# Performance work log

Measured on AMD Instinct MI355X. Metric: run time of the kernel, lower is better.

The kernel has to match this reference:

```python
import jax, jax.numpy as jnp
import numpy as np

# --- static config / quantization scales (simulating the torch-int modules) ---
B, S, E, H = 2, 2048, 2048, 16
D = E // H  # head_dim = 128
CATTN_ALPHA = 0.004   # W8A8B8O8Conv1D requant scale: int32 acc -> int8 out
QK_ALPHA = 1e-4       # BMM_S8T_S8N_F32T: s_q * s_k dequant scale -> fp32 logits
PV_ALPHA = 0.002      # BMM_S8T_S8N_S8T: (1/127)*s_v/s_out requant scale -> int8 out
PROJ_ALPHA = 0.003    # W8A8BFP32OFP32Conv1D dequant scale -> fp32 out


def q8(x):
    """round + saturate to int8 range (values kept in float32)."""
    return jnp.clip(jnp.round(x), -128.0, 127.0)


def setup_inputs() -> dict:
    key = jax.random.key(0)
    k0, k1, k2, k3, k4 = jax.random.split(key, 5)
    i8 = lambda k, shape: jax.random.randint(k, shape, -128, 128).astype(jnp.float32)
    return {
        "hidden_states": i8(k0, (B, S, E)),      # int8 activations (simulated)
        "w_attn": i8(k1, (E, 3 * E)),            # int8 c_attn weight (Conv1D: x @ W)
        "b_attn": i8(k2, (3 * E,)),              # int8 c_attn bias
        "w_proj": i8(k3, (E, E)),                # int8 c_proj weight
        "b_proj": jax.random.normal(k4, (E,), dtype=jnp.float32),  # fp32 c_proj bias
    }


def reference(hidden_states, w_attn, b_attn, w_proj, b_proj):
    # c_attn: W8A8B8O8 — int32 accumulate, requantize, add int8 bias, saturate
    qkv = q8(CATTN_ALPHA * jnp.matmul(hidden_states, w_attn) + b_attn)  # [B,S,3E] int8
    q, k, v = jnp.split(qkv, 3, axis=-1)

    def split_heads(t):  # [B,S,E] -> [B,H,S,D]
        return t.reshape(B, S, H, D).transpose(0, 2, 1, 3)

    q, k, v = split_heads(q), split_heads(k), split_heads(v)

    # qk_bmm: BMM_S8T_S8N_F32T -> fp32 logits, then /sqrt(head_dim)
    logits = QK_ALPHA * jnp.einsum("bhqd,bhkd->bhqk", q, k)
    logits = logits / jnp.float32(np.sqrt(D))

    # causal mask (tril bias buffer); masked positions -> dtype min
    causal = jnp.tril(jnp.ones((S, S), dtype=bool))
    mask_value = jnp.finfo(logits.dtype).min
    logits = jnp.where(causal[None, None], logits, mask_value)

    # softmax, then requantize probabilities to int8: round(p * 127)
    p = jax.nn.softmax(logits, axis=-1)
    p_i8 = q8(p * 127.0)  # [B,H,S,S] int8 (simulated)

    # pv_bmm: BMM_S8T_S8N_S8T -> int8 attn output
    attn_out = q8(PV_ALPHA * jnp.einsum("bhqk,bhkd->bhqd", p_i8, v))  # [B,H,S,D]

    # merge heads -> [B,S,E]
    attn_out = attn_out.transpose(0, 2, 1, 3).reshape(B, S, E)

    # c_proj: W8A8BFP32OFP32 — int32 accumulate, dequant to fp32, add fp32 bias
    out = PROJ_ALPHA * jnp.matmul(attn_out, w_proj) + b_proj  # [B,S,E] fp32
    return out
```

## Files before the change

### kernel.cpp

```cpp
#include <hip/hip_runtime.h>
#include <cstdint>
#include <cstddef>


typedef int v4i __attribute__((ext_vector_type(4)));

static constexpr float CATTN_ALPHA = 0.004f;
static constexpr float PV_ALPHA    = 0.002f;
static constexpr float PROJ_ALPHA  = 0.003f;
static constexpr float CE2   = 1.275174308e-05f;
static constexpr float MAGIC = 12582912.0f;

#define GLL16(gp, lp)                                              \
  __builtin_amdgcn_global_load_lds(                                \
      (const __attribute__((address_space(1))) void*)(gp),         \
      (__attribute__((address_space(3))) void*)(lp), 16, 0, 0)

__device__ __forceinline__ float exp2_fast(float x) {
#if __has_builtin(__builtin_amdgcn_exp2f)
  return __builtin_amdgcn_exp2f(x);
#else
  return __builtin_exp2f(x);
#endif
}

__device__ __forceinline__ uint32_t pack4(uint32_t u0, uint32_t u1, uint32_t u2,
                                          uint32_t u3) {
#if __has_builtin(__builtin_amdgcn_perm)
  uint32_t t01 = __builtin_amdgcn_perm(u1, u0, 0x00000400u);
  uint32_t t23 = __builtin_amdgcn_perm(u3, u2, 0x00000400u);
  return __builtin_amdgcn_perm(t23, t01, 0x05040100u);
#else
  return (u0 & 255u) | ((u1 & 255u) << 8) | ((u2 & 255u) << 16) | (u3 << 24);
#endif
}

__device__ __forceinline__ uint32_t rq8(float alpha, int a, float b) {
  float f = __fadd_rn(__fmul_rn(alpha, (float)a), b);
  f = rintf(f);
  f = fminf(fmaxf(f, -128.f), 127.f);
  return (uint32_t)((int)f) & 255u;
}

__global__ __launch_bounds__(256) void quant_kernel(const float* __restrict__ src,
                                                    int8_t* __restrict__ dst, int n4) {
  int i = blockIdx.x * 256 + threadIdx.x;
  if (i >= n4) return;
  float4 v = reinterpret_cast<const float4*>(src)[i];
  int b0 = __float2int_rn(v.x) & 255;
  int b1 = __float2int_rn(v.y) & 255;
  int b2 = __float2int_rn(v.z) & 255;
  int b3 = __float2int_rn(v.w) & 255;
  reinterpret_cast<int*>(dst)[i] = b0 | (b1 << 8) | (b2 << 16) | (b3 << 24);
}

__global__ __launch_bounds__(256) void quant_transpose_kernel(const float* __restrict__ src,
                                                              int8_t* __restrict__ dst,
                                                              int K, int N) {
  __shared__ int8_t ts[64][68];
  const int k0 = blockIdx.x * 64, n0 = blockIdx.y * 64;
  const int t = threadIdx.x;
  for (int c = t; c < 1024; c += 256) {
    int r = c >> 4, cc = (c & 15) << 2;
    float4 v = *reinterpret_cast<const float4*>(&src[(size_t)(k0 + r) * N + n0 + cc]);
    int b0 = __float2int_rn(v.x) & 255;
    int b1 = __float2int_rn(v.y) & 255;
    int b2 = __float2int_rn(v.z) & 255;
    int b3 = __float2int_rn(v.w) & 255;
    *reinterpret_cast<int*>(&ts[r][cc]) = b0 | (b1 << 8) | (b2 << 16) | (b3 << 24);
  }
  __syncthreads();
  {
    int c = t;
    int rn = c >> 2, ck = (c & 3) << 4;
    __attribute__((aligned(16))) int8_t tmp[16];
#pragma unroll
    for (int j = 0; j < 16; ++j) tmp[j] = ts[ck + j][rn];
    *reinterpret_cast<v4i*>(&dst[(size_t)(n0 + rn) * K + k0 + ck]) =
        *reinterpret_cast<const v4i*>(tmp);
  }
}

__global__ __launch_bounds__(256) void gemm_cattn_kernel(
    const int8_t* __restrict__ A, const int8_t* __restrict__ BT,
    const float* __restrict__ bias,
    int8_t* __restrict__ qout, int8_t* __restrict__ kout, int8_t* __restrict__ vtout) {
  __shared__ __align__(16) int8_t As[2][128][64];
  __shared__ __align__(16) int8_t Bs[2][128][64];
  const int t = threadIdx.x;
  const int lane = t & 63, wave = t >> 6;
  const int wr = wave >> 1, wc = wave & 1;
  const int l15 = lane & 15, l4 = lane >> 4;
  const int m0 = blockIdx.y * 128, n0 = blockIdx.x * 128;

  const int srow = lane >> 2;
  const int scol = (((lane & 3) ^ ((lane >> 3) & 3)) << 4);
  const int8_t* ag = A + (size_t)(m0 + wave * 32 + srow) * 2048 + scol;
  const int8_t* bg = BT + (size_t)(n0 + wave * 32 + srow) * 2048 + scol;

  auto stage = [&](int b, int ki) {
    const int8_t* a_ = ag + ki * 64;
    GLL16(a_, &As[b][wave * 32][0]);
    GLL16(a_ + (size_t)16 * 2048, &As[b][wave * 32 + 16][0]);
    const int8_t* b_ = bg + ki * 64;
    GLL16(b_, &Bs[b][wave * 32][0]);
    GLL16(b_ + (size_t)16 * 2048, &Bs[b][wave * 32 + 16][0]);
  };

  v4i acc[4][4];
#pragma unroll
  for (int i = 0; i < 4; ++i)
#pragma unroll
    for (int j = 0; j < 4; ++j) acc[i][j] = (v4i){0, 0, 0, 0};

  const int rsz = ((l4 ^ ((l15 >> 1) & 3)) << 4);
  const int aoff = (wr * 64 + l15) * 64 + rsz;
  const int boff = (wc * 64 + l15) * 64 + rsz;

  stage(0, 0);
  for (int ki = 0; ki < 32; ++ki) {
    if (ki < 31) {
      stage((ki + 1) & 1, ki + 1);
      asm volatile("s_waitcnt vmcnt(4)" ::: "memory");
    } else {
      asm volatile("s_waitcnt vmcnt(0)" ::: "memory");
    }
    __builtin_amdgcn_sched_barrier(0);
    __builtin_amdgcn_s_barrier();
    __builtin_amdgcn_sched_barrier(0);
    const int8_t* ab = &As[ki & 1][0][0];
    const int8_t* bb = &Bs[ki & 1][0][0];
    v4i af[4], bf[4];
#pragma unroll
    for (int i = 0; i < 4; ++i)
      af[i] = *reinterpret_cast<const v4i*>(ab + aoff + i * 1024);
#pragma unroll
    for (int j = 0; j < 4; ++j)
      bf[j] = *reinterpret_cast<const v4i*>(bb + boff + j * 1024);
#pragma unroll
    for (int i = 0; i < 4; ++i)
#pragma unroll
      for (int j = 0; j < 4; ++j)
        acc[i][j] = __builtin_amdgcn_mfma_i32_16x16x64_i8(af[i], bf[j], acc[i][j], 0, 0, 0);
    __builtin_amdgcn_sched_barrier(0);
    __builtin_amdgcn_s_barrier();
  }

  const int which = n0 >> 11;
  const int hh = (n0 & 2047) >> 7;
  const int bi = m0 >> 11;
  const int s_base = m0 & 2047;
  float bv[4];
#pragma unroll
  for (int j = 0; j < 4; ++j) bv[j] = bias[n0 + wc * 64 + j * 16 + l15];

  if (which == 2) {
    int8_t* vb = vtout + ((size_t)(bi * 16 + hh) * 128) * 2048;
#pragma unroll
    for (int i = 0; i < 4; ++i) {
#pragma unroll
      for (int j = 0; j < 4; ++j) {
        uint32_t w = pack4(rq8(CATTN_ALPHA, acc[i][j][0], bv[j]),
                           rq8(CATTN_ALPHA, acc[i][j][1], bv[j]),
                           rq8(CATTN_ALPHA, acc[i][j][2], bv[j]),
                           rq8(CATTN_ALPHA, acc[i][j][3], bv[j]));
        int d = wc * 64 + j * 16 + l15;
        int s0i = s_base + wr * 64 + i * 16 + l4 * 4;
        *reinterpret_cast<uint32_t*>(vb + (size_t)d * 2048 + s0i) = w;
      }
    }
  } else {
    int8_t* dst = (which == 0) ? qout : kout;
    int8_t* db = dst + ((size_t)(bi * 16 + hh) * 2048 + s_base) * 128;
#pragma unroll
    for (int i = 0; i < 4; ++i)
#pragma unroll
      for (int j = 0; j < 4; ++j)
#pragma unroll
        for (int rr = 0; rr < 4; ++rr) {
          float f = __fadd_rn(__fmul_rn(CATTN_ALPHA, (float)acc[i][j][rr]), bv[j]);
          f = rintf(f);
          f = fminf(fmaxf(f, -128.f), 127.f);
          int mo = wr * 64 + i * 16 + l4 * 4 + rr;
          int d = wc * 64 + j * 16 + l15;
          db[(size_t)mo * 128 + d] = (int8_t)(int)f;
        }
  }
}

__global__ __launch_bounds__(256) void gemm_cproj_kernel(
    const int8_t* __restrict__ A, const int8_t* __restrict__ BT,
    const float* __restrict__ bias, float* __restrict__ out) {
  __shared__ __align__(16) int8_t As[2][128][128];
  __shared__ __align__(16) int8_t Bs[2][128][128];
  const int t = threadIdx.x;
  const int lane = t & 63, wave = t >> 6;
  const int wr = wave >> 1, wc = wave & 1;
  const int l15 = lane & 15, l4 = lane >> 4;
  const int m0 = blockIdx.y * 128, n0 = blockIdx.x * 128;

  const int srow = lane >> 3;
  const int scol = ((lane & 7) ^ srow) << 4;
  const int8_t* ag = A + (size_t)(m0 + wave * 32 + srow) * 2048 + scol;
  const int8_t* bg = BT + (size_t)(n0 + wave * 32 + srow) * 2048 + scol;

  auto stage = [&](int b, int ki) {
    const int8_t* a_ = ag + ki * 128;
    const int8_t* b_ = bg + ki * 128;
#pragma unroll
    for (int g = 0; g < 4; ++g) {
      GLL16(a_ + (size_t)(g * 8) * 2048, &As[b][wave * 32 + g * 8][0]);
      GLL16(b_ + (size_t)(g * 8) * 2048, &Bs[b][wave * 32 + g * 8][0]);
    }
  };

  v4i acc[4][4];
#pragma unroll
  for (int i = 0; i < 4; ++i)
#pragma unroll
    for (int j = 0; j < 4; ++j) acc[i][j] = (v4i){0, 0, 0, 0};

  const int rswz = (l4 ^ (l15 & 7)) << 4;
  const int aoff = (wr * 64 + l15) * 128 + rswz;
  const int boff = (wc * 64 + l15) * 128 + rswz;

  stage(0, 0);
  for (int ki = 0; ki < 16; ++ki) {
    if (ki < 15) {
      stage((ki + 1) & 1, ki + 1);
      asm volatile("s_waitcnt vmcnt(8)" ::: "memory");
    } else {
      asm volatile("s_waitcnt vmcnt(0)" ::: "memory");
    }
    __builtin_amdgcn_sched_barrier(0);
    __builtin_amdgcn_s_barrier();
    __builtin_amdgcn_sched_barrier(0);
    const int8_t* ab = &As[ki & 1][0][0];
    const int8_t* bb = &Bs[ki & 1][0][0];
#pragma unroll
    for (int ks = 0; ks < 2; ++ks) {
      v4i af[4], bf[4];
#pragma unroll
      for (int i = 0; i < 4; ++i)
        af[i] = *reinterpret_cast<const v4i*>(ab + ((aoff + i * 2048) ^ (ks * 64)));
#pragma unroll
      for (int j = 0; j < 4; ++j)
        bf[j] = *reinterpret_cast<const v4i*>(bb + ((boff + j * 2048) ^ (ks * 64)));
#pragma unroll
      for (int i = 0; i < 4; ++i)
#pragma unroll
        for (int j = 0; j < 4; ++j)
          acc[i][j] = __builtin_amdgcn_mfma_i32_16x16x64_i8(bf[j], af[i], acc[i][j], 0, 0, 0);
    }
    __builtin_amdgcn_sched_barrier(0);
    __builtin_amdgcn_s_barrier();
  }
#pragma unroll
  for (int j = 0; j < 4; ++j) {
    float4 b4 = *reinterpret_cast<const float4*>(&bias[n0 + wc * 64 + j * 16 + l4 * 4]);
#pragma unroll
    for (int i = 0; i < 4; ++i) {
      int m = m0 + wr * 64 + i * 16 + l15;
      int n = n0 + wc * 64 + j * 16 + l4 * 4;
      float4 o;
      o.x = __fadd_rn(__fmul_rn(PROJ_ALPHA, (float)acc[i][j][0]), b4.x);
      o.y = __fadd_rn(__fmul_rn(PROJ_ALPHA, (float)acc[i][j][1]), b4.y);
      o.z = __fadd_rn(__fmul_rn(PROJ_ALPHA, (float)acc[i][j][2]), b4.z);
      o.w = __fadd_rn(__fmul_rn(PROJ_ALPHA, (float)acc[i][j][3]), b4.w);
      *reinterpret_cast<float4*>(&out[(size_t)m * 2048 + n]) = o;
    }
  }
}

__global__ __launch_bounds__(256) void attn_kernel(
    const int8_t* __restrict__ Q, const int8_t* __restrict__ K8,
    const int8_t* __restrict__ VT, int8_t* __restrict__ O) {
  __shared__ __align__(16) int8_t q_s[64][128];
  __shared__ __align__(16) int8_t k_s[2][64][128];
  __shared__ __align__(16) int8_t vt_s[2][128][64];
  __shared__ __align__(16) int8_t p_s[64][80];

  const int t = threadIdx.x;
  const int lane = t & 63, wave = t >> 6;
  const int l15 = lane & 15, l4 = lane >> 4;
  const int bh = blockIdx.x;
  const int qt = (int)gridDim.y - 1 - (int)blockIdx.y;
  const int r0 = qt * 64;
  const size_t kqbase = (size_t)bh * (2048 * 128);
  const size_t vtbase = (size_t)bh * (128 * 2048);

  const int kq_go = ((lane >> 3) << 7) + ((((lane & 7) ^ (lane >> 3)) & 7) << 4);
  const int vt_go = ((lane >> 2) * 2048) + ((lane & 3) << 4);
  const int koff0 = (l15 << 7) + ((((0 + l4) ^ l15) & 7) << 4);
  const int koff1 = (l15 << 7) + ((((4 + l4) ^ l15) & 7) << 4);
  const int voff = l15 * 64 + l4 * 16;
  const int poff_w = (wave * 16 + l15) * 80 + l4 * 4;
  const int poff_r = (wave * 16 + l15) * 80 + l4 * 16;

  {
    const int8_t* qg = Q + kqbase + (size_t)(r0 + wave * 16) * 128 + kq_go;
    GLL16(qg, &q_s[wave * 16][0]);
    GLL16(qg + 8 * 128, &q_s[wave * 16 + 8][0]);
    const int8_t* kg = K8 + kqbase + (size_t)(wave * 16) * 128 + kq_go;
    GLL16(kg, &k_s[0][wave * 16][0]);
    GLL16(kg + 8 * 128, &k_s[0][wave * 16 + 8][0]);
  }
  __syncthreads();

  const v4i qf0 = *reinterpret_cast<const v4i*>(&q_s[0][0] + wave * 2048 + koff0);
  const v4i qf1 = *reinterpret_cast<const v4i*>(&q_s[0][0] + wave * 2048 + koff1);
  const int qgl = wave * 16 + l15;

  float acc_l[4] = {0.f, 0.f, 0.f, 0.f};

  for (int tt = 0; tt <= qt; ++tt) {
    if (tt < qt) {
      const int8_t* kg =
          K8 + kqbase + (size_t)((tt + 1) * 64 + wave * 16) * 128 + kq_go;
      GLL16(kg, &k_s[(tt + 1) & 1][wave * 16][0]);
      GLL16(kg + 8 * 128, &k_s[(tt + 1) & 1][wave * 16 + 8][0]);
    }
    const int8_t* kb = &k_s[tt & 1][0][0];
    v4i sacc[4];
#pragma unroll
    for (int ni = 0; ni < 4; ++ni) sacc[ni] = (v4i){0, 0, 0, 0};
#pragma unroll
    for (int ni = 0; ni < 4; ++ni) {
      v4i ak = *reinterpret_cast<const v4i*>(kb + ni * 2048 + koff0);
      sacc[ni] = __builtin_amdgcn_mfma_i32_16x16x64_i8(ak, qf0, sacc[ni], 0, 0, 0);
    }
#pragma unroll
    for (int ni = 0; ni < 4; ++ni) {
      v4i ak = *reinterpret_cast<const v4i*>(kb + ni * 2048 + koff1);
      sacc[ni] = __builtin_amdgcn_mfma_i32_16x16x64_i8(ak, qf1, sacc[ni], 0, 0, 0);
    }
    if (tt < qt) {
#pragma unroll
      for (int ni = 0; ni < 4; ++ni)
#pragma unroll
        for (int rr = 0; rr < 4; ++rr)
          acc_l[rr] += exp2_fast(CE2 * (float)sacc[ni][rr]);
    } else {
#pragma unroll
      for (int ni = 0; ni < 4; ++ni)
#pragma unroll
        for (int rr = 0; rr < 4; ++rr) {
          float e = exp2_fast(CE2 * (float)sacc[ni][rr]);
          acc_l[rr] += (ni * 16 + l4 * 4 + rr <= qgl) ? e : 0.f;
        }
    }
    __syncthreads();
  }
  float l_run = (acc_l[0] + acc_l[1]) + (acc_l[2] + acc_l[3]);
  l_run += __shfl_xor(l_run, 16);
  l_run += __shfl_xor(l_run, 32);
  const float inv = 127.0f / l_run;

  {
    const int8_t* kg = K8 + kqbase + (size_t)(wave * 16) * 128 + kq_go;
    GLL16(kg, &k_s[0][wave * 16][0]);
    GLL16(kg + 8 * 128, &k_s[0][wave * 16 + 8][0]);
    const int8_t* vg = VT + vtbase + (size_t)(wave * 32) * 2048 + vt_go;
    GLL16(vg, &vt_s[0][wave * 32][0]);
    GLL16(vg + (size_t)16 * 2048, &vt_s[0][wave * 32 + 16][0]);
  }
  __syncthreads();

  v4i oacc[8];
#pragma unroll
  for (int nj = 0; nj < 8; ++nj) oacc[nj] = (v4i){0, 0, 0, 0};

  for (int tt = 0; tt <= qt; ++tt) {
    if (tt < qt) {
      const int kb1 = (tt + 1) * 64;
      const int8_t* kg = K8 + kqbase + (size_t)(kb1 + wave * 16) * 128 + kq_go;
      GLL16(kg, &k_s[(tt + 1) & 1][wave * 16][0]);
      GLL16(kg + 8 * 128, &k_s[(tt + 1) & 1][wave * 16 + 8][0]);
      const int8_t* vg = VT + vtbase + (size_t)(wave * 32) * 2048 + kb1 + vt_go;
      GLL16(vg, &vt_s[(tt + 1) & 1][wave * 32][0]);
      GLL16(vg + (size_t)16 * 2048, &vt_s[(tt + 1) & 1][wave * 32 + 16][0]);
    }
    const int8_t* kb = &k_s[tt & 1][0][0];
    v4i sacc[4];
#pragma unroll
    for (int ni = 0; ni < 4; ++ni) sacc[ni] = (v4i){0, 0, 0, 0};
#pragma unroll
    for (int ni = 0; ni < 4; ++ni) {
      v4i ak = *reinterpret_cast<const v4i*>(kb + ni * 2048 + koff0);
      sacc[ni] = __builtin_amdgcn_mfma_i32_16x16x64_i8(ak, qf0, sacc[ni], 0, 0, 0);
    }
#pragma unroll
    for (int ni = 0; ni < 4; ++ni) {
      v4i ak = *reinterpret_cast<const v4i*>(kb + ni * 2048 + koff1);
      sacc[ni] = __builtin_amdgcn_mfma_i32_16x16x64_i8(ak, qf1, sacc[ni], 0, 0, 0);
    }
    if (tt < qt) {
#pragma unroll
      for (int ni = 0; ni < 4; ++ni) {
        float f0 = fmaf(exp2_fast(CE2 * (float)sacc[ni][0]), inv, MAGIC);
        float f1 = fmaf(exp2_fast(CE2 * (float)sacc[ni][1]), inv, MAGIC);
        float f2 = fmaf(exp2_fast(CE2 * (float)sacc[ni][2]), inv, MAGIC);
        float f3 = fmaf(exp2_fast(CE2 * (float)sacc[ni][3]), inv, MAGIC);
        uint32_t w = pack4(__float_as_uint(f0), __float_as_uint(f1),
                           __float_as_uint(f2), __float_as_uint(f3));
        *reinterpret_cast<uint32_t*>(&p_s[0][0] + poff_w + ni * 16) = w;
      }
    } else {
#pragma unroll
      for (int ni = 0; ni < 4; ++ni) {
        float e0 = exp2_fast(CE2 * (float)sacc[ni][0]);
        float e1 = exp2_fast(CE2 * (float)sacc[ni][1]);
        float e2 = exp2_fast(CE2 * (float)sacc[ni][2]);
        float e3 = exp2_fast(CE2 * (float)sacc[ni][3]);
        int c = ni * 16 + l4 * 4;
        e0 = (c + 0 <= qgl) ? e0 : 0.f;
        e1 = (c + 1 <= qgl) ? e1 : 0.f;
        e2 = (c + 2 <= qgl) ? e2 : 0.f;
        e3 = (c + 3 <= qgl) ? e3 : 0.f;
        float f0 = fmaf(e0, inv, MAGIC), f1 = fmaf(e1, inv, MAGIC);
        float f2 = fmaf(e2, inv, MAGIC), f3 = fmaf(e3, inv, MAGIC);
        uint32_t w = pack4(__float_as_uint(f0), __float_as_uint(f1),
                           __float_as_uint(f2), __float_as_uint(f3));
        *reinterpret_cast<uint32_t*>(&p_s[0][0] + poff_w + ni * 16) = w;
      }
    }
    asm volatile("s_waitcnt lgkmcnt(0)" ::: "memory");
    v4i pf = *reinterpret_cast<const v4i*>(&p_s[0][0] + poff_r);
    const int8_t* vb = &vt_s[tt & 1][0][0];
#pragma unroll
    for (int nj = 0; nj < 8; ++nj) {
      v4i vf = *reinterpret_cast<const v4i*>(vb + nj * 1024 + voff);
      oacc[nj] = __builtin_amdgcn_mfma_i32_16x16x64_i8(vf, pf, oacc[nj], 0, 0, 0);
    }
    __syncthreads();
  }

  const int bq = bh >> 4, hh = bh & 15;
  {
    int r = r0 + wave * 16 + l15;
    int8_t* ob = O + ((size_t)bq * 2048 + r) * 2048 + hh * 128;
#pragma unroll
    for (int nj = 0; nj < 8; ++nj) {
      uint32_t w = pack4(rq8(PV_ALPHA, oacc[nj][0], 0.f),
                         rq8(PV_ALPHA, oacc[nj][1], 0.f),
                         rq8(PV_ALPHA, oacc[nj][2], 0.f),
                         rq8(PV_ALPHA, oacc[nj][3], 0.f));
      *reinterpret_cast<uint32_t*>(ob + nj * 16 + l4 * 4) = w;
    }
  }
}

extern "C" void kernel_launch(void* const* d_in, const int* in_sizes, int n_in,
                              void* d_out, int out_size, void* d_ws, size_t ws_size,
                              hipStream_t stream) {
  const float* hs_f    = (const float*)d_in[0];
  const float* wattn_f = (const float*)d_in[1];
  const float* battn_f = (const float*)d_in[2];
  const float* wproj_f = (const float*)d_in[3];
  const float* bproj_f = (const float*)d_in[4];
  float* out_f = (float*)d_out;

  int8_t* ws = (int8_t*)d_ws;
  int8_t* hs_i8   = ws;
  int8_t* wT_attn = ws + 8388608;
  int8_t* wT_proj = ws + 20971520;
  int8_t* q_i8    = ws + 25165824;
  int8_t* k_i8    = ws + 33554432;
  int8_t* vT_i8   = ws + 41943040;
  int8_t* attn_i8 = ws + 50331648;

  quant_kernel<<<dim3(8192), dim3(256), 0, stream>>>(hs_f, hs_i8, 2097152);
  quant_transpose_kernel<<<dim3(32, 96), dim3(256), 0, stream>>>(wattn_f, wT_attn, 2048, 6144);
  quant_transpose_kernel<<<dim3(32, 32), dim3(256), 0, stream>>>(wproj_f, wT_proj, 2048, 2048);
  gemm_cattn_kernel<<<dim3(48, 32), dim3(256), 0, stream>>>(hs_i8, wT_attn, battn_f,
                                                            q_i8, k_i8, vT_i8);
  attn_kernel<<<dim3(32, 32), dim3(256), 0, stream>>>(q_i8, k_i8, vT_i8, attn_i8);
  gemm_cproj_kernel<<<dim3(16, 32), dim3(256), 0, stream>>>(attn_i8, wT_proj, bproj_f, out_f);
}
```

Before: 186.3 us.

## Enlarge c_attn GEMM tile to 256x256 with 8 waves and ping-pong staging

The QKV projection GEMM moves from 128x128 tiles with 256 threads to 256x256 tiles with 512 threads and K-steps of 128. Loads of the next K tile are spread across four sub-phases, each separated by barriers, and MFMA bursts run at raised priority. The goal is higher arithmetic intensity per loaded byte and better overlap of global-to-LDS loads with MFMA work. The cost is 128KB of LDS and many more accumulators per thread, which lowers occupancy. The grid drops to 384 blocks, which may leave some CUs idle.

```diff
diff --git a/kernel.cpp b/kernel.cpp
--- a/kernel.cpp
+++ b/kernel.cpp
@@ -81,110 +81,171 @@
   }
 }
 
-__global__ __launch_bounds__(256) void gemm_cattn_kernel(
+__global__ __launch_bounds__(512) void gemm_cattn_kernel(
     const int8_t* __restrict__ A, const int8_t* __restrict__ BT,
     const float* __restrict__ bias,
     int8_t* __restrict__ qout, int8_t* __restrict__ kout, int8_t* __restrict__ vtout) {
-  __shared__ __align__(16) int8_t As[2][128][64];
-  __shared__ __align__(16) int8_t Bs[2][128][64];
+  __shared__ __align__(16) int8_t As[2][2][128][128];
+  __shared__ __align__(16) int8_t Bs[2][2][128][128];
   const int t = threadIdx.x;
-  const int lane = t & 63, wave = t >> 6;
-  const int wr = wave >> 1, wc = wave & 1;
+  const int lane = t & 63, w = t >> 6;
+  const int wr = w >> 2, wcn = w & 3;
   const int l15 = lane & 15, l4 = lane >> 4;
-  const int m0 = blockIdx.y * 128, n0 = blockIdx.x * 128;
-
-  const int srow = lane >> 2;
-  const int scol = (((lane & 3) ^ ((lane >> 3) & 3)) << 4);
-  const int8_t* ag = A + (size_t)(m0 + wave * 32 + srow) * 2048 + scol;
-  const int8_t* bg = BT + (size_t)(n0 + wave * 32 + srow) * 2048 + scol;
-
-  auto stage = [&](int b, int ki) {
-    const int8_t* a_ = ag + ki * 64;
-    GLL16(a_, &As[b][wave * 32][0]);
-    GLL16(a_ + (size_t)16 * 2048, &As[b][wave * 32 + 16][0]);
-    const int8_t* b_ = bg + ki * 64;
-    GLL16(b_, &Bs[b][wave * 32][0]);
-    GLL16(b_ + (size_t)16 * 2048, &Bs[b][wave * 32 + 16][0]);
+  const int m0 = blockIdx.y * 256, n0 = blockIdx.x * 256;
+
+  const int srow = lane >> 3;
+  const int scol = ((lane & 7) ^ srow) << 4;
+  const int8_t* ag = A + (size_t)(m0 + w * 16 + srow) * 2048 + scol;
+  const int8_t* bg = BT + (size_t)(n0 + w * 16 + srow) * 2048 + scol;
+
+  auto stageA = [&](int bb, int kt, int h) {
+    GLL16(ag + (size_t)(h * 128) * 2048 + kt, &As[bb][h][w * 16][0]);
+    GLL16(ag + (size_t)(h * 128 + 8) * 2048 + kt, &As[bb][h][w * 16 + 8][0]);
   };
-
-  v4i acc[4][4];
-#pragma unroll
-  for (int i = 0; i < 4; ++i)
-#pragma unroll
-    for (int j = 0; j < 4; ++j) acc[i][j] = (v4i){0, 0, 0, 0};
-
-  const int rsz = ((l4 ^ ((l15 >> 1) & 3)) << 4);
-  const int aoff = (wr * 64 + l15) * 64 + rsz;
-  const int boff = (wc * 64 + l15) * 64 + rsz;
-
-  stage(0, 0);
-  for (int ki = 0; ki < 32; ++ki) {
-    if (ki < 31) {
-      stage((ki + 1) & 1, ki + 1);
-      asm volatile("s_waitcnt vmcnt(4)" ::: "memory");
-    } else {
-      asm volatile("s_waitcnt vmcnt(0)" ::: "memory");
-    }
-    __builtin_amdgcn_sched_barrier(0);
-    __builtin_amdgcn_s_barrier();
-    __builtin_amdgcn_sched_barrier(0);
-    const int8_t* ab = &As[ki & 1][0][0];
-    const int8_t* bb = &Bs[ki & 1][0][0];
-    v4i af[4], bf[4];
+  auto stageB = [&](int bb, int kt, int h) {
+    GLL16(bg + (size_t)(h * 128) * 2048 + kt, &Bs[bb][h][w * 16][0]);
+    GLL16(bg + (size_t)(h * 128 + 8) * 2048 + kt, &Bs[bb][h][w * 16 + 8][0]);
+  };
+
+  v4i acc[2][4][2][2];
+#pragma unroll
+  for (int mh = 0; mh < 2; ++mh)
 #pragma unroll
     for (int i = 0; i < 4; ++i)
-      af[i] = *reinterpret_cast<const v4i*>(ab + aoff + i * 1024);
-#pragma unroll
-    for (int j = 0; j < 4; ++j)
-      bf[j] = *reinterpret_cast<const v4i*>(bb + boff + j * 1024);
-#pragma unroll
-    for (int i = 0; i < 4; ++i)
-#pragma unroll
-      for (int j = 0; j < 4; ++j)
-        acc[i][j] = __builtin_amdgcn_mfma_i32_16x16x64_i8(af[i], bf[j], acc[i][j], 0, 0, 0);
-    __builtin_amdgcn_sched_barrier(0);
-    __builtin_amdgcn_s_barrier();
+#pragma unroll
+      for (int nh = 0; nh < 2; ++nh)
+#pragma unroll
+        for (int j = 0; j < 2; ++j) acc[mh][i][nh][j] = (v4i){0, 0, 0, 0};
+
+  const int arsw = ((l4 ^ (l15 & 7)) << 4);
+  const int browoff = (wcn & 1) * 64;
+
+  stageA(0, 0, 0); stageA(0, 0, 1); stageB(0, 0, 0); stageB(0, 0, 1);
+
+  for (int kt16 = 0; kt16 < 16; ++kt16) {
+    const int bb = kt16 & 1;
+    const int8_t* ab = &As[bb][wr][0][0];
+    const int8_t* bbp = &Bs[bb][wcn >> 1][0][0];
+    const int ktn = (kt16 + 1) * 128;
+#pragma unroll
+    for (int p = 0; p < 4; ++p) {
+      const int mh = p >> 1, nh = p & 1;
+      v4i af[4][2], bf[2][2];
+      if (p == 0) {
+        if (kt16 < 15) {
+          stageA(bb ^ 1, ktn, 0);
+          asm volatile("s_waitcnt vmcnt(2)" ::: "memory");
+        } else {
+          asm volatile("s_waitcnt vmcnt(0)" ::: "memory");
+        }
+        __builtin_amdgcn_sched_barrier(0);
+        __builtin_amdgcn_s_barrier();
+        __builtin_amdgcn_sched_barrier(0);
+#pragma unroll
+        for (int i = 0; i < 4; ++i) {
+          int ro = (mh * 64 + i * 16 + l15) * 128 + arsw;
+#pragma unroll
+          for (int ks = 0; ks < 2; ++ks)
+            af[i][ks] = *reinterpret_cast<const v4i*>(ab + (ro ^ (ks * 64)));
+        }
+#pragma unroll
+        for (int j = 0; j < 2; ++j) {
+          int ro = (browoff + nh * 32 + j * 16 + l15) * 128 + arsw;
+#pragma unroll
+          for (int ks = 0; ks < 2; ++ks)
+            bf[j][ks] = *reinterpret_cast<const v4i*>(bbp + (ro ^ (ks * 64)));
+        }
+      } else {
+#pragma unroll
+        for (int i = 0; i < 4; ++i) {
+          int ro = (mh * 64 + i * 16 + l15) * 128 + arsw;
+#pragma unroll
+          for (int ks = 0; ks < 2; ++ks)
+            af[i][ks] = *reinterpret_cast<const v4i*>(ab + (ro ^ (ks * 64)));
+        }
+#pragma unroll
+        for (int j = 0; j < 2; ++j) {
+          int ro = (browoff + nh * 32 + j * 16 + l15) * 128 + arsw;
+#pragma unroll
+          for (int ks = 0; ks < 2; ++ks)
+            bf[j][ks] = *reinterpret_cast<const v4i*>(bbp + (ro ^ (ks * 64)));
+        }
+        if (kt16 < 15) {
+          if (p == 1) stageA(bb ^ 1, ktn, 1);
+          else if (p == 2) stageB(bb ^ 1, ktn, 0);
+          else stageB(bb ^ 1, ktn, 1);
+        }
+        __builtin_amdgcn_sched_barrier(0);
+        __builtin_amdgcn_s_barrier();
+        __builtin_amdgcn_sched_barrier(0);
+      }
+      asm volatile("s_waitcnt lgkmcnt(0)" ::: "memory");
+      __builtin_amdgcn_sched_barrier(0);
+      __builtin_amdgcn_s_setprio(1);
+#pragma unroll
+      for (int ks = 0; ks < 2; ++ks)
+#pragma unroll
+        for (int i = 0; i < 4; ++i)
+#pragma unroll
+          for (int j = 0; j < 2; ++j)
+            acc[mh][i][nh][j] = __builtin_amdgcn_mfma_i32_16x16x64_i8(
+                af[i][ks], bf[j][ks], acc[mh][i][nh][j], 0, 0, 0);
+      __builtin_amdgcn_s_setprio(0);
+      __builtin_amdgcn_sched_barrier(0);
+      __builtin_amdgcn_s_barrier();
+    }
   }
 
   const int which = n0 >> 11;
-  const int hh = (n0 & 2047) >> 7;
   const int bi = m0 >> 11;
   const int s_base = m0 & 2047;
-  float bv[4];
-#pragma unroll
-  for (int j = 0; j < 4; ++j) bv[j] = bias[n0 + wc * 64 + j * 16 + l15];
+  const int hh = ((n0 & 2047) >> 7) + (wcn >> 1);
+  float bv[2][2];
+#pragma unroll
+  for (int nh = 0; nh < 2; ++nh)
+#pragma unroll
+    for (int j = 0; j < 2; ++j)
+      bv[nh][j] = bias[n0 + wcn * 64 + nh * 32 + j * 16 + l15];
 
   if (which == 2) {
     int8_t* vb = vtout + ((size_t)(bi * 16 + hh) * 128) * 2048;
 #pragma unroll
-    for (int i = 0; i < 4; ++i) {
-#pragma unroll
-      for (int j = 0; j < 4; ++j) {
-        uint32_t w = pack4(rq8(CATTN_ALPHA, acc[i][j][0], bv[j]),
-                           rq8(CATTN_ALPHA, acc[i][j][1], bv[j]),
-                           rq8(CATTN_ALPHA, acc[i][j][2], bv[j]),
-                           rq8(CATTN_ALPHA, acc[i][j][3], bv[j]));
-        int d = wc * 64 + j * 16 + l15;
-        int s0i = s_base + wr * 64 + i * 16 + l4 * 4;
-        *reinterpret_cast<uint32_t*>(vb + (size_t)d * 2048 + s0i) = w;
-      }
-    }
+    for (int mh = 0; mh < 2; ++mh)
+#pragma unroll
+      for (int i = 0; i < 4; ++i)
+#pragma unroll
+        for (int nh = 0; nh < 2; ++nh)
+#pragma unroll
+          for (int j = 0; j < 2; ++j) {
+            uint32_t ww = pack4(rq8(CATTN_ALPHA, acc[mh][i][nh][j][0], bv[nh][j]),
+                                rq8(CATTN_ALPHA, acc[mh][i][nh][j][1], bv[nh][j]),
+                                rq8(CATTN_ALPHA, acc[mh][i][nh][j][2], bv[nh][j]),
+                                rq8(CATTN_ALPHA, acc[mh][i][nh][j][3], bv[nh][j]));
+            int d = (wcn & 1) * 64 + nh * 32 + j * 16 + l15;
+            int s0i = s_base + wr * 128 + mh * 64 + i * 16 + l4 * 4;
+            *reinterpret_cast<uint32_t*>(vb + (size_t)d * 2048 + s0i) = ww;
+          }
   } else {
     int8_t* dst = (which == 0) ? qout : kout;
     int8_t* db = dst + ((size_t)(bi * 16 + hh) * 2048 + s_base) * 128;
 #pragma unroll
-    for (int i = 0; i < 4; ++i)
-#pragma unroll
-      for (int j = 0; j < 4; ++j)
-#pragma unroll
-        for (int rr = 0; rr < 4; ++rr) {
-          float f = __fadd_rn(__fmul_rn(CATTN_ALPHA, (float)acc[i][j][rr]), bv[j]);
-          f = rintf(f);
-          f = fminf(fmaxf(f, -128.f), 127.f);
-          int mo = wr * 64 + i * 16 + l4 * 4 + rr;
-          int d = wc * 64 + j * 16 + l15;
-          db[(size_t)mo * 128 + d] = (int8_t)(int)f;
-        }
+    for (int mh = 0; mh < 2; ++mh)
+#pragma unroll
+      for (int i = 0; i < 4; ++i)
+#pragma unroll
+        for (int nh = 0; nh < 2; ++nh)
+#pragma unroll
+          for (int j = 0; j < 2; ++j)
+#pragma unroll
+            for (int rr = 0; rr < 4; ++rr) {
+              float f = __fadd_rn(
+                  __fmul_rn(CATTN_ALPHA, (float)acc[mh][i][nh][j][rr]), bv[nh][j]);
+              f = rintf(f);
+              f = fminf(fmaxf(f, -128.f), 127.f);
+              int mo = wr * 128 + mh * 64 + i * 16 + l4 * 4 + rr;
+              int d = (wcn & 1) * 64 + nh * 32 + j * 16 + l15;
+              db[(size_t)mo * 128 + d] = (int8_t)(int)f;
+            }
   }
 }
 
@@ -472,7 +533,7 @@
   quant_kernel<<<dim3(8192), dim3(256), 0, stream>>>(hs_f, hs_i8, 2097152);
   quant_transpose_kernel<<<dim3(32, 96), dim3(256), 0, stream>>>(wattn_f, wT_attn, 2048, 6144);
   quant_transpose_kernel<<<dim3(32, 32), dim3(256), 0, stream>>>(wproj_f, wT_proj, 2048, 2048);
-  gemm_cattn_kernel<<<dim3(48, 32), dim3(256), 0, stream>>>(hs_i8, wT_attn, battn_f,
+  gemm_cattn_kernel<<<dim3(24, 16), dim3(512), 0, stream>>>(hs_i8, wT_attn, battn_f,
                                                             q_i8, k_i8, vT_i8);
   attn_kernel<<<dim3(32, 32), dim3(256), 0, stream>>>(q_i8, k_i8, vT_i8, attn_i8);
   gemm_cproj_kernel<<<dim3(16, 32), dim3(256), 0, stream>>>(attn_i8, wT_proj, bproj_f, out_f);
```

Result: slower. 190.4 us (+2.2%).
